# Kernel tuning notes

Hardware: AMD Instinct MI355X
Metric: run time of the kernel (lower is better)

The kernel has to match this reference:

```python
import jax, jax.numpy as jnp
import numpy as np
from jax import lax

ALPHA = 0.3          # opt['retrieval_strategy']['margin']
NB_SAMPLES = 10      # hardest negatives kept per anchor
W_IRR = 1.0
W_RII = 1.0
B = 4096
D = 1024
NB_CLASSES = 1048


def _pairwise_dist(x, y):
    # Euclidean pairwise distance matrix [B, B] (self.dist in the torch module)
    x2 = jnp.sum(x * x, axis=1, keepdims=True)          # [B,1]
    y2 = jnp.sum(y * y, axis=1, keepdims=True).T        # [1,B]
    d2 = x2 + y2 - 2.0 * (x @ y.T)
    return jnp.sqrt(jnp.maximum(d2, 0.0))


def setup_inputs() -> dict:
    key = jax.random.key(0)
    k1, k2, k3, k4 = jax.random.split(key, 4)
    input1 = jax.random.normal(k1, (B, D), dtype=jnp.float32)
    input2 = jax.random.normal(k2, (B, D), dtype=jnp.float32)
    # target==1 everywhere -> 'matches' mask selects the whole batch (identity gather)
    target = jnp.ones((B, 1), dtype=jnp.int32)
    # classes in [1, NB_CLASSES) -> all rows valid (class != 0)
    class1 = jax.random.randint(k3, (B, 1), 1, NB_CLASSES, dtype=jnp.int32)
    class2 = jax.random.randint(k4, (B, 1), 1, NB_CLASSES, dtype=jnp.int32)
    return {"input1": input1, "input2": input2, "target": target,
            "class1": class1, "class2": class2}


def _mine(cost):
    # calculate_cost with sampling='max_negative': sort rows descending, keep nb_samples.
    # top_k == descending sort truncated to k.
    top, _ = lax.top_k(cost, NB_SAMPLES)                # [B, NB_SAMPLES]
    return top


def reference(input1, input2, target, class1, class2):
    # matches = (target == 1) is all-true by construction -> instance_* = full inputs
    dist = _pairwise_dist(input1, input2)               # [B, B]
    diag = jnp.diagonal(dist)                           # [B]
    n = dist.shape[0]
    eye = jnp.eye(n, dtype=bool)

    # IRR: anchor image, positive its own recipe, negatives other recipes
    cost_irr = jnp.maximum(diag[:, None] - dist + ALPHA, 0.0)
    cost_irr = jnp.where(eye, 0.0, cost_irr)
    top_irr = _mine(cost_irr)
    bad_irr = jnp.mean((top_irr == 0.0).astype(jnp.float32))
    loss_irr = top_irr.mean() * W_IRR

    # RII: anchor recipe, positive its own image, negatives other images (cost.t())
    cost_rii = jnp.maximum(diag[None, :] - dist + ALPHA, 0.0)
    cost_rii = jnp.where(eye, 0.0, cost_rii)
    top_rii = _mine(cost_rii.T)
    bad_rii = jnp.mean((top_rii == 0.0).astype(jnp.float32))
    loss_rii = top_rii.mean() * W_RII

    return jnp.stack([loss_irr, loss_rii, bad_irr, bad_rii])
```

## Files before the change

kernel.cpp:

```cpp
#include <hip/hip_runtime.h>
#include <hip/hip_fp16.h>

#define ALPHA 0.3f
#define B_SZ 4096
#define D_SZ 1024
#define CT_STRIDE 132
#define BIGF 3.0e38f
#define SENT_F 60000.0f

typedef __attribute__((ext_vector_type(8))) _Float16 half8;
typedef __attribute__((ext_vector_type(4))) _Float16 half4;
typedef __attribute__((ext_vector_type(2))) _Float16 half2v;
typedef __attribute__((ext_vector_type(4))) float floatx4;

typedef __attribute__((address_space(1))) const void* gas_t;
typedef __attribute__((address_space(3))) void* las_t;

__device__ __forceinline__ float wave_reduce_add(float v) {
#pragma unroll
    for (int off = 32; off; off >>= 1) v += __shfl_xor(v, off);
    return v;
}

__device__ __forceinline__ void insert10(float (&best)[10], float x) {
#pragma unroll
    for (int p = 0; p < 10; ++p) {
        float lo = fminf(best[p], x);
        x = fmaxf(best[p], x);
        best[p] = lo;
    }
}

__device__ __forceinline__ void insert10p(half2v (&b)[10], half2v x) {
#pragma unroll
    for (int p = 0; p < 10; ++p) {
        half2v lo = __builtin_elementwise_min(b[p], x);
        x = __builtin_elementwise_max(b[p], x);
        b[p] = lo;
    }
}

__global__ void __launch_bounds__(256) prep_kernel(
    const float* __restrict__ in1, const float* __restrict__ in2,
    _Float16* __restrict__ Xh, _Float16* __restrict__ Yh,
    float* __restrict__ x2, float* __restrict__ y2, float* __restrict__ mth) {
    int row = blockIdx.x;
    int t = threadIdx.x;
    const float4* a4 = (const float4*)(in1 + (size_t)row * D_SZ);
    const float4* b4 = (const float4*)(in2 + (size_t)row * D_SZ);
    float4 a = a4[t], b = b4[t];
    half4 ha = {(_Float16)a.x, (_Float16)a.y, (_Float16)a.z, (_Float16)a.w};
    half4 hb = {(_Float16)b.x, (_Float16)b.y, (_Float16)b.z, (_Float16)b.w};
    ((half4*)(Xh + (size_t)row * D_SZ))[t] = ha;
    ((half4*)(Yh + (size_t)row * D_SZ))[t] = hb;
    float sa = a.x * a.x + a.y * a.y + a.z * a.z + a.w * a.w;
    float sb = b.x * b.x + b.y * b.y + b.z * b.z + b.w * b.w;
    float d0 = a.x - b.x, d1 = a.y - b.y, d2v = a.z - b.z, d3 = a.w - b.w;
    float sd = d0 * d0 + d1 * d1 + d2v * d2v + d3 * d3;
    sa = wave_reduce_add(sa);
    sb = wave_reduce_add(sb);
    sd = wave_reduce_add(sd);
    __shared__ float red[3][4];
    int wave = t >> 6, lane = t & 63;
    if (lane == 0) { red[0][wave] = sa; red[1][wave] = sb; red[2][wave] = sd; }
    __syncthreads();
    if (t == 0) {
        x2[row] = red[0][0] + red[0][1] + red[0][2] + red[0][3];
        y2[row] = red[1][0] + red[1][1] + red[1][2] + red[1][3];
        mth[row] = sqrtf(red[2][0] + red[2][1] + red[2][2] + red[2][3]) + ALPHA;
    }
}

__global__ void __launch_bounds__(256, 4) gemm_topk_kernel(
    const _Float16* __restrict__ Xh, const _Float16* __restrict__ Yh,
    const float* __restrict__ x2, const float* __restrict__ y2,
    _Float16* __restrict__ CandI, _Float16* __restrict__ CandR) {
    __shared__ _Float16 smem[16896];
    _Float16* As = smem;
    _Float16* Bs = smem + 4096;
    int tid = threadIdx.x;
    int wave = tid >> 6, lane = tid & 63;
    int waveR = wave >> 1, waveC = wave & 1;
    int id = blockIdx.y * 32 + blockIdx.x;
    int st = id >> 6, w = id & 63;
    int bx = (st & 3) * 8 + (w & 7);
    int by = (st >> 2) * 8 + (w >> 3);
    int q = lane >> 4, mrow = lane & 15;

    floatx4 acc[4][4] = {};

    int c0 = tid, c1 = 256 + tid;
    int r0 = c0 >> 2, q0 = (c0 & 3) ^ ((r0 >> 1) & 3);
    int r1 = c1 >> 2, q1 = (c1 & 3) ^ ((r1 >> 1) & 3);
    const _Float16* gA0 = Xh + (size_t)(by * 128 + r0) * D_SZ + q0 * 8;
    const _Float16* gB0 = Yh + (size_t)(bx * 128 + r0) * D_SZ + q0 * 8;
    const _Float16* gA1 = Xh + (size_t)(by * 128 + r1) * D_SZ + q1 * 8;
    const _Float16* gB1 = Yh + (size_t)(bx * 128 + r1) * D_SZ + q1 * 8;
    _Float16* la0 = &As[(wave * 64) * 8];
    _Float16* lb0 = &Bs[(wave * 64) * 8];
    _Float16* la1 = &As[(256 + wave * 64) * 8];
    _Float16* lb1 = &Bs[(256 + wave * 64) * 8];

    int aoff[4], boff[4];
#pragma unroll
    for (int mi = 0; mi < 4; ++mi) {
        int R = waveR * 64 + mi * 16 + mrow;
        aoff[mi] = R * 32 + (q ^ ((R >> 1) & 3)) * 8;
    }
#pragma unroll
    for (int ni = 0; ni < 4; ++ni) {
        int R = waveC * 64 + ni * 16 + mrow;
        boff[ni] = R * 32 + (q ^ ((R >> 1) & 3)) * 8;
    }

    for (int k0 = 0; k0 < D_SZ; k0 += 32) {
        __syncthreads();
        __builtin_amdgcn_global_load_lds((gas_t)(const void*)(gA0 + k0), (las_t)(void*)la0, 16, 0, 0);
        __builtin_amdgcn_global_load_lds((gas_t)(const void*)(gB0 + k0), (las_t)(void*)lb0, 16, 0, 0);
        __builtin_amdgcn_global_load_lds((gas_t)(const void*)(gA1 + k0), (las_t)(void*)la1, 16, 0, 0);
        __builtin_amdgcn_global_load_lds((gas_t)(const void*)(gB1 + k0), (las_t)(void*)lb1, 16, 0, 0);
        __syncthreads();
        half8 af[4], bf[4];
#pragma unroll
        for (int mi = 0; mi < 4; ++mi) af[mi] = *(const half8*)&As[aoff[mi]];
#pragma unroll
        for (int ni = 0; ni < 4; ++ni) bf[ni] = *(const half8*)&Bs[boff[ni]];
#pragma unroll
        for (int mi = 0; mi < 4; ++mi)
#pragma unroll
            for (int ni = 0; ni < 4; ++ni)
                acc[mi][ni] = __builtin_amdgcn_mfma_f32_16x16x32_f16(af[mi], bf[ni], acc[mi][ni], 0, 0, 0);
    }
    __syncthreads();

    _Float16* Ct = smem;
#pragma unroll
    for (int ni = 0; ni < 4; ++ni) {
        int lc = waveC * 64 + ni * 16 + mrow;
        float y2v = y2[bx * 128 + lc];
#pragma unroll
        for (int mi = 0; mi < 4; ++mi) {
            int lr0 = waveR * 64 + mi * 16 + q * 4;
            int gr0 = by * 128 + lr0;
            floatx4 v = acc[mi][ni];
            half4 hv = {(_Float16)(x2[gr0 + 0] + y2v - 2.0f * v[0]),
                        (_Float16)(x2[gr0 + 1] + y2v - 2.0f * v[1]),
                        (_Float16)(x2[gr0 + 2] + y2v - 2.0f * v[2]),
                        (_Float16)(x2[gr0 + 3] + y2v - 2.0f * v[3])};
            *(half4*)&Ct[lc * CT_STRIDE + lr0] = hv;
        }
    }
    __syncthreads();
    if (bx == by && tid < 128) Ct[tid * CT_STRIDE + tid] = (_Float16)SENT_F;
    __syncthreads();

    const half2v sent2 = {(_Float16)SENT_F, (_Float16)SENT_F};

    if (wave < 2) {
        int p = wave * 32 + (lane & 31);
        int chalf = lane >> 5;
        half2v b[10];
#pragma unroll
        for (int i = 0; i < 10; ++i) b[i] = sent2;
#pragma unroll 8
        for (int i = 0; i < 64; ++i) {
            int c = chalf * 64 + i;
            half2v v = *(const half2v*)&Ct[c * CT_STRIDE + 2 * p];
            insert10p(b, v);
        }
        half2v t[10];
#pragma unroll
        for (int k = 0; k < 10; ++k)
            t[k] = __builtin_bit_cast(half2v, __shfl_xor(__builtin_bit_cast(int, b[k]), 32));
#pragma unroll
        for (int k = 0; k < 10; ++k) insert10p(b, t[k]);
        if (lane < 32) {
            int grow = by * 128 + 2 * p;
            unsigned int* d0 = (unsigned int*)CandI + ((size_t)grow * 32 + bx) * 5;
            unsigned int* d1 = d0 + 32 * 5;
#pragma unroll
            for (int k = 0; k < 5; ++k) {
                unsigned int u0 = __builtin_bit_cast(unsigned int, b[2 * k]);
                unsigned int u1 = __builtin_bit_cast(unsigned int, b[2 * k + 1]);
                d0[k] = (u0 & 0xFFFFu) | (u1 << 16);
                d1[k] = (u0 >> 16) | (u1 & 0xFFFF0000u);
            }
        }
    } else {
        int c = (wave - 2) * 64 + lane;
        half2v b[10];
#pragma unroll
        for (int i = 0; i < 10; ++i) b[i] = sent2;
        const half2v* colp = (const half2v*)&Ct[c * CT_STRIDE];
#pragma unroll 8
        for (int i = 0; i < 64; ++i) insert10p(b, colp[i]);
        half2v sw[10];
#pragma unroll
        for (int k = 0; k < 10; ++k) {
            unsigned int u = __builtin_bit_cast(unsigned int, b[k]);
            sw[k] = __builtin_bit_cast(half2v, (u >> 16) | (u << 16));
        }
#pragma unroll
        for (int k = 0; k < 10; ++k) insert10p(b, sw[k]);
        int gcol = bx * 128 + c;
        unsigned int* d = (unsigned int*)CandR + ((size_t)gcol * 32 + by) * 5;
#pragma unroll
        for (int k = 0; k < 5; ++k) {
            unsigned int u0 = __builtin_bit_cast(unsigned int, b[2 * k]);
            unsigned int u1 = __builtin_bit_cast(unsigned int, b[2 * k + 1]);
            d[k] = (u0 & 0xFFFFu) | (u1 << 16);
        }
    }
}

__global__ void __launch_bounds__(256) merge_kernel(
    const _Float16* __restrict__ CandI, const _Float16* __restrict__ CandR,
    const float* __restrict__ mth,
    float* __restrict__ Srow, float* __restrict__ Zrow) {
    int wave = threadIdx.x >> 6, lane = threadIdx.x & 63;
    int r = blockIdx.x * 4 + wave;
    int row = r & (B_SZ - 1);
    const _Float16* cp = ((r < B_SZ) ? CandI : CandR) + (size_t)row * 320;
    float best[10];
#pragma unroll
    for (int i = 0; i < 10; ++i) best[i] = BIGF;
#pragma unroll
    for (int j = 0; j < 5; ++j) insert10(best, (float)cp[j * 64 + lane]);

    float mrow = mth[row];
    float s = 0.f, z = 0.f;
#pragma unroll
    for (int round = 0; round < 10; ++round) {
        float v0 = best[0];
        float g = v0;
#pragma unroll
        for (int off = 32; off; off >>= 1) g = fminf(g, __shfl_xor(g, off));
        unsigned long long ball = __ballot(v0 == g);
        int leader = __ffsll(ball) - 1;
        if (lane == leader) {
#pragma unroll
            for (int p = 0; p < 9; ++p) best[p] = best[p + 1];
            best[9] = BIGF;
        }
        float d = sqrtf(fmaxf(g, 0.f));
        float c = fmaxf(mrow - d, 0.f);
        s += c;
        z += (c == 0.f) ? 1.f : 0.f;
    }
    if (lane == 0) { Srow[r] = s; Zrow[r] = z; }
}

__global__ void __launch_bounds__(256) finalize_kernel(
    const float* __restrict__ Srow, const float* __restrict__ Zrow,
    float* __restrict__ out) {
    __shared__ float red[256][4];
    int t = threadIdx.x;
    float s0 = 0, s1 = 0, z0 = 0, z1 = 0;
#pragma unroll
    for (int k = 0; k < 8; ++k) {
        int i = k * 256 + t;
        float4 sv = ((const float4*)Srow)[i];
        float4 zv = ((const float4*)Zrow)[i];
        float ss = sv.x + sv.y + sv.z + sv.w;
        float zz = zv.x + zv.y + zv.z + zv.w;
        if (i < 1024) { s0 += ss; z0 += zz; } else { s1 += ss; z1 += zz; }
    }
    red[t][0] = s0; red[t][1] = s1; red[t][2] = z0; red[t][3] = z1;
    __syncthreads();
    for (int off = 128; off > 0; off >>= 1) {
        if (t < off) {
#pragma unroll
            for (int j = 0; j < 4; ++j) red[t][j] += red[t + off][j];
        }
        __syncthreads();
    }
    if (t == 0) {
        const float inv = 1.0f / (float)(B_SZ * 10);
        out[0] = red[0][0] * inv;
        out[1] = red[0][1] * inv;
        out[2] = red[0][2] * inv;
        out[3] = red[0][3] * inv;
    }
}

extern "C" void kernel_launch(void* const* d_in, const int* in_sizes, int n_in,
                              void* d_out, int out_size, void* d_ws, size_t ws_size,
                              hipStream_t stream) {
    const float* in1 = (const float*)d_in[0];
    const float* in2 = (const float*)d_in[1];
    float* out = (float*)d_out;

    char* ws = (char*)d_ws;
    const size_t MB = 1024 * 1024;
    _Float16* Xh = (_Float16*)(ws);
    _Float16* Yh = (_Float16*)(ws + 8 * MB);
    _Float16* CandI = (_Float16*)(ws + 16 * MB);
    _Float16* CandR = (_Float16*)(ws + 19 * MB);
    float* x2   = (float*)(ws + 22 * MB);
    float* y2   = x2 + B_SZ;
    float* mth  = y2 + B_SZ;
    float* Srow = mth + B_SZ;
    float* Zrow = Srow + 2 * B_SZ;
    const size_t needed = 22 * MB + (size_t)(3 * B_SZ + 4 * B_SZ) * sizeof(float);
    if (ws_size < needed) return;

    hipLaunchKernelGGL(prep_kernel, dim3(B_SZ), dim3(256), 0, stream,
                       in1, in2, Xh, Yh, x2, y2, mth);
    hipLaunchKernelGGL(gemm_topk_kernel, dim3(32, 32), dim3(256), 0, stream,
                       Xh, Yh, x2, y2, CandI, CandR);
    hipLaunchKernelGGL(merge_kernel, dim3(2048), dim3(256), 0, stream,
                       CandI, CandR, mth, Srow, Zrow);
    hipLaunchKernelGGL(finalize_kernel, dim3(1), dim3(256), 0, stream,
                       Srow, Zrow, out);
}
```

Baseline: 144.3 us.

## Quantize inputs to FP8 and run pairwise-distance GEMM with FP8 MFMA

The prep kernel now packs the inputs into FP8 bytes instead of FP16, and the GEMM uses the fp8 16x16x32 MFMA with a K step of 64 and a byte-based swizzled LDS layout. This halves global and LDS traffic for the operands and uses the higher-throughput FP8 matrix path. Norms and the diagonal are still computed in fp32. The cost is much lower precision in the cross terms, which can change which negatives land in the top-k and near-zero margins. The launch-bounds occupancy hint was also dropped.

```diff
diff --git a/kernel.cpp b/kernel.cpp
--- a/kernel.cpp
+++ b/kernel.cpp
@@ -8,7 +8,6 @@
 #define BIGF 3.0e38f
 #define SENT_F 60000.0f
 
-typedef __attribute__((ext_vector_type(8))) _Float16 half8;
 typedef __attribute__((ext_vector_type(4))) _Float16 half4;
 typedef __attribute__((ext_vector_type(2))) _Float16 half2v;
 typedef __attribute__((ext_vector_type(4))) float floatx4;
@@ -42,17 +41,20 @@
 
 __global__ void __launch_bounds__(256) prep_kernel(
     const float* __restrict__ in1, const float* __restrict__ in2,
-    _Float16* __restrict__ Xh, _Float16* __restrict__ Yh,
+    unsigned char* __restrict__ Xq, unsigned char* __restrict__ Yq,
     float* __restrict__ x2, float* __restrict__ y2, float* __restrict__ mth) {
     int row = blockIdx.x;
     int t = threadIdx.x;
     const float4* a4 = (const float4*)(in1 + (size_t)row * D_SZ);
     const float4* b4 = (const float4*)(in2 + (size_t)row * D_SZ);
     float4 a = a4[t], b = b4[t];
-    half4 ha = {(_Float16)a.x, (_Float16)a.y, (_Float16)a.z, (_Float16)a.w};
-    half4 hb = {(_Float16)b.x, (_Float16)b.y, (_Float16)b.z, (_Float16)b.w};
-    ((half4*)(Xh + (size_t)row * D_SZ))[t] = ha;
-    ((half4*)(Yh + (size_t)row * D_SZ))[t] = hb;
+    int ua = 0, ub = 0;
+    ua = __builtin_amdgcn_cvt_pk_fp8_f32(a.x, a.y, ua, false);
+    ua = __builtin_amdgcn_cvt_pk_fp8_f32(a.z, a.w, ua, true);
+    ub = __builtin_amdgcn_cvt_pk_fp8_f32(b.x, b.y, ub, false);
+    ub = __builtin_amdgcn_cvt_pk_fp8_f32(b.z, b.w, ub, true);
+    ((int*)(Xq + (size_t)row * D_SZ))[t] = ua;
+    ((int*)(Yq + (size_t)row * D_SZ))[t] = ub;
     float sa = a.x * a.x + a.y * a.y + a.z * a.z + a.w * a.w;
     float sb = b.x * b.x + b.y * b.y + b.z * b.z + b.w * b.w;
     float d0 = a.x - b.x, d1 = a.y - b.y, d2v = a.z - b.z, d3 = a.w - b.w;
@@ -71,13 +73,13 @@
     }
 }
 
-__global__ void __launch_bounds__(256, 4) gemm_topk_kernel(
-    const _Float16* __restrict__ Xh, const _Float16* __restrict__ Yh,
+__global__ void __launch_bounds__(256) gemm_topk_kernel(
+    const unsigned char* __restrict__ Xq, const unsigned char* __restrict__ Yq,
     const float* __restrict__ x2, const float* __restrict__ y2,
     _Float16* __restrict__ CandI, _Float16* __restrict__ CandR) {
-    __shared__ _Float16 smem[16896];
-    _Float16* As = smem;
-    _Float16* Bs = smem + 4096;
+    __shared__ __align__(16) unsigned char smem[33792];
+    unsigned char* As = smem;
+    unsigned char* Bs = smem + 8192;
     int tid = threadIdx.x;
     int wave = tid >> 6, lane = tid & 63;
     int waveR = wave >> 1, waveC = wave & 1;
@@ -89,51 +91,58 @@
 
     floatx4 acc[4][4] = {};
 
-    int c0 = tid, c1 = 256 + tid;
-    int r0 = c0 >> 2, q0 = (c0 & 3) ^ ((r0 >> 1) & 3);
-    int r1 = c1 >> 2, q1 = (c1 & 3) ^ ((r1 >> 1) & 3);
-    const _Float16* gA0 = Xh + (size_t)(by * 128 + r0) * D_SZ + q0 * 8;
-    const _Float16* gB0 = Yh + (size_t)(bx * 128 + r0) * D_SZ + q0 * 8;
-    const _Float16* gA1 = Xh + (size_t)(by * 128 + r1) * D_SZ + q1 * 8;
-    const _Float16* gB1 = Yh + (size_t)(bx * 128 + r1) * D_SZ + q1 * 8;
-    _Float16* la0 = &As[(wave * 64) * 8];
-    _Float16* lb0 = &Bs[(wave * 64) * 8];
-    _Float16* la1 = &As[(256 + wave * 64) * 8];
-    _Float16* lb1 = &Bs[(256 + wave * 64) * 8];
-
-    int aoff[4], boff[4];
+    const unsigned char* srcA[2];
+    const unsigned char* srcB[2];
+    unsigned char* dstA[2];
+    unsigned char* dstB[2];
+#pragma unroll
+    for (int i = 0; i < 2; ++i) {
+        int c = i * 256 + tid;
+        int r = c >> 2, u = c & 3;
+        int g = u ^ ((r >> 1) & 3);
+        srcA[i] = Xq + (size_t)(by * 128 + r) * D_SZ + g * 16;
+        srcB[i] = Yq + (size_t)(bx * 128 + r) * D_SZ + g * 16;
+        dstA[i] = As + (i * 256 + wave * 64) * 16;
+        dstB[i] = Bs + (i * 256 + wave * 64) * 16;
+    }
+
+    int aoff[2][4], boff[2][4];
 #pragma unroll
     for (int mi = 0; mi < 4; ++mi) {
-        int R = waveR * 64 + mi * 16 + mrow;
-        aoff[mi] = R * 32 + (q ^ ((R >> 1) & 3)) * 8;
-    }
-#pragma unroll
-    for (int ni = 0; ni < 4; ++ni) {
-        int R = waveC * 64 + ni * 16 + mrow;
-        boff[ni] = R * 32 + (q ^ ((R >> 1) & 3)) * 8;
-    }
-
-    for (int k0 = 0; k0 < D_SZ; k0 += 32) {
+        int Ra = waveR * 64 + mi * 16 + mrow;
+        int Rb = waveC * 64 + mi * 16 + mrow;
+#pragma unroll
+        for (int ks = 0; ks < 2; ++ks) {
+            int u = ks * 2 + (q >> 1);
+            aoff[ks][mi] = Ra * 64 + (u ^ ((Ra >> 1) & 3)) * 16 + (q & 1) * 8;
+            boff[ks][mi] = Rb * 64 + (u ^ ((Rb >> 1) & 3)) * 16 + (q & 1) * 8;
+        }
+    }
+
+    for (int k0 = 0; k0 < D_SZ; k0 += 64) {
         __syncthreads();
-        __builtin_amdgcn_global_load_lds((gas_t)(const void*)(gA0 + k0), (las_t)(void*)la0, 16, 0, 0);
-        __builtin_amdgcn_global_load_lds((gas_t)(const void*)(gB0 + k0), (las_t)(void*)lb0, 16, 0, 0);
-        __builtin_amdgcn_global_load_lds((gas_t)(const void*)(gA1 + k0), (las_t)(void*)la1, 16, 0, 0);
-        __builtin_amdgcn_global_load_lds((gas_t)(const void*)(gB1 + k0), (las_t)(void*)lb1, 16, 0, 0);
+        __builtin_amdgcn_global_load_lds((gas_t)(const void*)(srcA[0] + k0), (las_t)(void*)dstA[0], 16, 0, 0);
+        __builtin_amdgcn_global_load_lds((gas_t)(const void*)(srcB[0] + k0), (las_t)(void*)dstB[0], 16, 0, 0);
+        __builtin_amdgcn_global_load_lds((gas_t)(const void*)(srcA[1] + k0), (las_t)(void*)dstA[1], 16, 0, 0);
+        __builtin_amdgcn_global_load_lds((gas_t)(const void*)(srcB[1] + k0), (las_t)(void*)dstB[1], 16, 0, 0);
         __syncthreads();
-        half8 af[4], bf[4];
-#pragma unroll
-        for (int mi = 0; mi < 4; ++mi) af[mi] = *(const half8*)&As[aoff[mi]];
-#pragma unroll
-        for (int ni = 0; ni < 4; ++ni) bf[ni] = *(const half8*)&Bs[boff[ni]];
-#pragma unroll
-        for (int mi = 0; mi < 4; ++mi)
-#pragma unroll
-            for (int ni = 0; ni < 4; ++ni)
-                acc[mi][ni] = __builtin_amdgcn_mfma_f32_16x16x32_f16(af[mi], bf[ni], acc[mi][ni], 0, 0, 0);
-    }
-    __syncthreads();
-
-    _Float16* Ct = smem;
+#pragma unroll
+        for (int ks = 0; ks < 2; ++ks) {
+            long af[4], bf[4];
+#pragma unroll
+            for (int mi = 0; mi < 4; ++mi) af[mi] = *(const long*)&As[aoff[ks][mi]];
+#pragma unroll
+            for (int ni = 0; ni < 4; ++ni) bf[ni] = *(const long*)&Bs[boff[ks][ni]];
+#pragma unroll
+            for (int mi = 0; mi < 4; ++mi)
+#pragma unroll
+                for (int ni = 0; ni < 4; ++ni)
+                    acc[mi][ni] = __builtin_amdgcn_mfma_f32_16x16x32_fp8_fp8(af[mi], bf[ni], acc[mi][ni], 0, 0, 0);
+        }
+    }
+    __syncthreads();
+
+    _Float16* Ct = (_Float16*)smem;
 #pragma unroll
     for (int ni = 0; ni < 4; ++ni) {
         int lc = waveC * 64 + ni * 16 + mrow;
@@ -292,22 +301,22 @@
 
     char* ws = (char*)d_ws;
     const size_t MB = 1024 * 1024;
-    _Float16* Xh = (_Float16*)(ws);
-    _Float16* Yh = (_Float16*)(ws + 8 * MB);
-    _Float16* CandI = (_Float16*)(ws + 16 * MB);
-    _Float16* CandR = (_Float16*)(ws + 19 * MB);
-    float* x2   = (float*)(ws + 22 * MB);
+    unsigned char* Xq = (unsigned char*)(ws);
+    unsigned char* Yq = (unsigned char*)(ws + 4 * MB);
+    _Float16* CandI = (_Float16*)(ws + 8 * MB);
+    _Float16* CandR = (_Float16*)(ws + 11 * MB);
+    float* x2   = (float*)(ws + 14 * MB);
     float* y2   = x2 + B_SZ;
     float* mth  = y2 + B_SZ;
     float* Srow = mth + B_SZ;
     float* Zrow = Srow + 2 * B_SZ;
-    const size_t needed = 22 * MB + (size_t)(3 * B_SZ + 4 * B_SZ) * sizeof(float);
+    const size_t needed = 14 * MB + (size_t)(3 * B_SZ + 4 * B_SZ) * sizeof(float);
     if (ws_size < needed) return;
 
     hipLaunchKernelGGL(prep_kernel, dim3(B_SZ), dim3(256), 0, stream,
-                       in1, in2, Xh, Yh, x2, y2, mth);
+                       in1, in2, Xq, Yq, x2, y2, mth);
     hipLaunchKernelGGL(gemm_topk_kernel, dim3(32, 32), dim3(256), 0, stream,
-                       Xh, Yh, x2, y2, CandI, CandR);
+                       Xq, Yq, x2, y2, CandI, CandR);
     hipLaunchKernelGGL(merge_kernel, dim3(2048), dim3(256), 0, stream,
                        CandI, CandR, mth, Srow, Zrow);
     hipLaunchKernelGGL(finalize_kernel, dim3(1), dim3(256), 0, stream,
```

Result: faster. 132.6 us (-8.1%).
